# Kernel tuning notes

Hardware: AMD Instinct MI355X
Metric: run time of the kernel (lower is better)

The kernel has to match this reference:

```python
import jax, jax.numpy as jnp
import numpy as np

B, N, DIM = 2, 1024, 256
DEPTH, HEADS, DIM_HEAD = 4, 4, 64
INNER = HEADS * DIM_HEAD
SCALE = DIM_HEAD ** -0.5
STEP, LAMBD, EPS = 0.1, 0.1, 1e-5


def cx(re, im):
    return jax.lax.complex(re, im)


def setup_inputs() -> dict:
    key = jax.random.key(0)
    ks = jax.random.split(key, 8)
    s = np.float32(1.0 / np.sqrt(DIM))
    f32 = jnp.float32
    return {
        "x_re": jax.random.normal(ks[0], (B, N, DIM), f32),
        "x_im": jax.random.normal(ks[1], (B, N, DIM), f32),
        "ln1_w_re": jnp.ones((DEPTH, DIM), f32),
        "ln1_w_im": jnp.zeros((DEPTH, DIM), f32),
        "ln1_b_re": jnp.zeros((DEPTH, DIM), f32),
        "ln1_b_im": jnp.zeros((DEPTH, DIM), f32),
        "qkv_re": jax.random.normal(ks[2], (DEPTH, INNER, DIM), f32) * s,
        "qkv_im": jax.random.normal(ks[3], (DEPTH, INNER, DIM), f32) * s,
        "out_w_re": jax.random.normal(ks[4], (DEPTH, DIM, INNER), f32) * s,
        "out_w_im": jax.random.normal(ks[5], (DEPTH, DIM, INNER), f32) * s,
        "out_b_re": jnp.zeros((DEPTH, DIM), f32),
        "out_b_im": jnp.zeros((DEPTH, DIM), f32),
        "ln2_w_re": jnp.ones((DEPTH, DIM), f32),
        "ln2_w_im": jnp.zeros((DEPTH, DIM), f32),
        "ln2_b_re": jnp.zeros((DEPTH, DIM), f32),
        "ln2_b_im": jnp.zeros((DEPTH, DIM), f32),
        "ff_re": jax.random.normal(ks[6], (DEPTH, DIM, DIM), f32) * s,
        "ff_im": jax.random.normal(ks[7], (DEPTH, DIM, DIM), f32) * s,
    }


def complex_layernorm(x, w, b):
    # per-component mean/var on real and imag (torch unbiased=False), complex sqrt
    mean = cx(jnp.mean(x.real, -1, keepdims=True), jnp.mean(x.imag, -1, keepdims=True))
    var = cx(jnp.var(x.real, -1, keepdims=True), jnp.var(x.imag, -1, keepdims=True))
    xn = (x - mean) / jnp.sqrt(var + EPS)
    return w * xn + b


def attention(x, Wqkv, Wout, bout):
    # torch Linear: y = x @ W^T ; shared qkv projection w
    w = jnp.einsum('bnd,ed->bne', x, Wqkv)              # [B,N,INNER]
    w = w.reshape(B, N, HEADS, DIM_HEAD).transpose(0, 2, 1, 3)  # [B,H,N,Dh]
    dots = jnp.einsum('bhnd,bhmd->bhnm', w, w.conj()) * SCALE   # complex scores
    mag = jnp.abs(dots)
    a = jax.nn.softmax(mag, axis=-1)                    # softmax on magnitudes
    ph = jnp.angle(dots)                                # polar reconstruction
    attn = cx(a * jnp.cos(ph), a * jnp.sin(ph))
    out = jnp.einsum('bhnm,bhmd->bhnd', attn, w)
    out = out.transpose(0, 2, 1, 3).reshape(B, N, INNER)
    return jnp.einsum('bne,de->bnd', out, Wout) + bout


def feedforward(x, W):
    # FeedForward type1: x1 = x W^T ; CReLU(x + step*x1 - step*lambd)
    x1 = jnp.einsum('bnd,ed->bne', x, W)
    z = x + STEP * x1 - STEP * LAMBD
    return cx(jax.nn.relu(z.real), jax.nn.relu(z.imag))


def reference(x_re, x_im, ln1_w_re, ln1_w_im, ln1_b_re, ln1_b_im,
              qkv_re, qkv_im, out_w_re, out_w_im, out_b_re, out_b_im,
              ln2_w_re, ln2_w_im, ln2_b_re, ln2_b_im, ff_re, ff_im):
    x = cx(x_re, x_im)
    for l in range(DEPTH):
        xn = complex_layernorm(x, cx(ln1_w_re[l], ln1_w_im[l]), cx(ln1_b_re[l], ln1_b_im[l]))
        grad_x = attention(xn, cx(qkv_re[l], qkv_im[l]), cx(out_w_re[l], out_w_im[l]),
                           cx(out_b_re[l], out_b_im[l])) + x
        xn2 = complex_layernorm(grad_x, cx(ln2_w_re[l], ln2_w_im[l]), cx(ln2_b_re[l], ln2_b_im[l]))
        x = feedforward(xn2, cx(ff_re[l], ff_im[l]))
    return x
```

## Files before the change

### kernel.cpp

```cpp
#include <hip/hip_runtime.h>
#include <math.h>

#define B_ 2
#define N_ 1024
#define DIM_ 256
#define DEPTH_ 4
#define HEADS_ 4
#define DHEAD_ 64
#define INNER_ 256
#define SCALE_ 0.125f
#define STEP_ 0.1f
#define LAMBD_ 0.1f
#define EPS_ 1e-5f

typedef __attribute__((ext_vector_type(8))) short short8;
typedef __attribute__((ext_vector_type(4))) float f32x4;

__device__ __forceinline__ unsigned short bf16_rne(float x) {
    unsigned u = __float_as_uint(x);
    unsigned r = (u + 0x7FFFu + ((u >> 16) & 1u)) >> 16;
    return (unsigned short)r;
}
__device__ __forceinline__ float bf16_tof(unsigned short h) {
    return __uint_as_float(((unsigned)h) << 16);
}
__device__ __forceinline__ void split2(float x, unsigned short& hi, unsigned short& lo) {
    hi = bf16_rne(x);
    lo = bf16_rne(x - bf16_tof(hi));
}
__device__ __forceinline__ f32x4 mfma16(short8 a, short8 b, f32x4 c) {
    return __builtin_amdgcn_mfma_f32_16x16x32_bf16(a, b, c, 0, 0, 0);
}
__device__ __forceinline__ short8 neg8(short8 v) {
    union { short8 s; unsigned u[4]; } a; a.s = v;
    a.u[0] ^= 0x80008000u; a.u[1] ^= 0x80008000u;
    a.u[2] ^= 0x80008000u; a.u[3] ^= 0x80008000u;
    return a.s;
}

__global__ __launch_bounds__(64)
void ln_kernel(const float* __restrict__ xr, const float* __restrict__ xi,
               const float* __restrict__ wr, const float* __restrict__ wi,
               const float* __restrict__ br, const float* __restrict__ bi,
               float* __restrict__ outr, float* __restrict__ outi,
               unsigned short* __restrict__ planes, int S) {
    int row = blockIdx.x;
    int lane = threadIdx.x;
    int base = row * DIM_ + lane * 4;

    float4 xr4 = *(const float4*)(xr + base);
    float4 xi4 = *(const float4*)(xi + base);
    float ar[4] = {xr4.x, xr4.y, xr4.z, xr4.w};
    float ai[4] = {xi4.x, xi4.y, xi4.z, xi4.w};

    float sr = ar[0] + ar[1] + ar[2] + ar[3];
    float si = ai[0] + ai[1] + ai[2] + ai[3];
#pragma unroll
    for (int o = 1; o < 64; o <<= 1) {
        sr += __shfl_xor(sr, o, 64);
        si += __shfl_xor(si, o, 64);
    }
    float mre = sr * (1.f / DIM_), mim = si * (1.f / DIM_);

    float drv[4], div[4];
    float vr = 0.f, vi = 0.f;
#pragma unroll
    for (int j = 0; j < 4; j++) {
        drv[j] = ar[j] - mre;
        div[j] = ai[j] - mim;
        vr += drv[j] * drv[j];
        vi += div[j] * div[j];
    }
#pragma unroll
    for (int o = 1; o < 64; o <<= 1) {
        vr += __shfl_xor(vr, o, 64);
        vi += __shfl_xor(vi, o, 64);
    }
    float c = vr * (1.f / DIM_) + EPS_;
    float d = vi * (1.f / DIM_);
    float r = sqrtf(c * c + d * d);
    float sre = sqrtf(0.5f * (r + c));
    float sim = sqrtf(fmaxf(0.5f * (r - c), 0.f));
    float inv = 1.f / r;

    int wc = lane * 4;
    float4 wr4 = *(const float4*)(wr + wc);
    float4 wi4 = *(const float4*)(wi + wc);
    float4 br4 = *(const float4*)(br + wc);
    float4 bi4 = *(const float4*)(bi + wc);
    float wrv[4] = {wr4.x, wr4.y, wr4.z, wr4.w};
    float wiv[4] = {wi4.x, wi4.y, wi4.z, wi4.w};
    float brv[4] = {br4.x, br4.y, br4.z, br4.w};
    float biv[4] = {bi4.x, bi4.y, bi4.z, bi4.w};

    float orr[4], oii[4];
    unsigned short rh[4], rl[4], ih[4], il[4];
#pragma unroll
    for (int j = 0; j < 4; j++) {
        float nr = (drv[j] * sre + div[j] * sim) * inv;
        float ni = (div[j] * sre - drv[j] * sim) * inv;
        orr[j] = wrv[j] * nr - wiv[j] * ni + brv[j];
        oii[j] = wrv[j] * ni + wiv[j] * nr + biv[j];
        split2(orr[j], rh[j], rl[j]);
        split2(oii[j], ih[j], il[j]);
    }
    *(float4*)(outr + base) = make_float4(orr[0], orr[1], orr[2], orr[3]);
    *(float4*)(outi + base) = make_float4(oii[0], oii[1], oii[2], oii[3]);
    *(ushort4*)(planes + 0 * (size_t)S + base) = make_ushort4(rh[0], rh[1], rh[2], rh[3]);
    *(ushort4*)(planes + 1 * (size_t)S + base) = make_ushort4(rl[0], rl[1], rl[2], rl[3]);
    *(ushort4*)(planes + 2 * (size_t)S + base) = make_ushort4(ih[0], ih[1], ih[2], ih[3]);
    *(ushort4*)(planes + 3 * (size_t)S + base) = make_ushort4(il[0], il[1], il[2], il[3]);
}

__global__ void wsplit_all(const float* __restrict__ s0r, const float* __restrict__ s0i,
                           const float* __restrict__ s1r, const float* __restrict__ s1i,
                           const float* __restrict__ s2r, const float* __restrict__ s2i,
                           unsigned short* __restrict__ d0,
                           unsigned short* __restrict__ d1,
                           unsigned short* __restrict__ d2) {
    const int PER = DEPTH_ * 65536;
    int gid = blockIdx.x * 256 + threadIdx.x;
    int sel = gid / PER;
    int idx = gid - sel * PER;
    const float* wr = (sel == 0) ? s0r : (sel == 1) ? s1r : s2r;
    const float* wi = (sel == 0) ? s0i : (sel == 1) ? s1i : s2i;
    unsigned short* dst = (sel == 0) ? d0 : (sel == 1) ? d1 : d2;
    int l = idx >> 16, e = idx & 65535;
    unsigned short rh, rl, ih, il;
    split2(wr[idx], rh, rl);
    split2(wi[idx], ih, il);
    size_t base = (size_t)l * 4 * 65536;
    dst[base + 0 * 65536 + e] = rh;
    dst[base + 1 * 65536 + e] = rl;
    dst[base + 2 * 65536 + e] = ih;
    dst[base + 3 * 65536 + e] = il;
}

template <int MODE>
__global__ __launch_bounds__(64)
void gemm_mfma(const unsigned short* __restrict__ Ap, int aStride,
               const unsigned short* __restrict__ Bp,
               unsigned short* __restrict__ wpo, unsigned short* __restrict__ wtpo,
               const float* __restrict__ biasR, const float* __restrict__ biasI,
               const float* resR, const float* resI,
               float* xoR, float* xoI, int S) {
    const int K = 256;
    int tileM = blockIdx.x * 16, tileN = blockIdx.y * 16;
    int lane = threadIdx.x;
    int m16 = lane & 15, quad = lane >> 4;

    f32x4 accP = (f32x4){0,0,0,0}, accN = (f32x4){0,0,0,0};
    f32x4 accIa = (f32x4){0,0,0,0}, accIb = (f32x4){0,0,0,0};

#pragma unroll
    for (int k0 = 0; k0 < 256; k0 += 32) {
        int kb = k0 + quad * 8;
        short8 a[4], b[4];
#pragma unroll
        for (int p = 0; p < 4; p++) {
            a[p] = *(const short8*)(Ap + (size_t)p * aStride + (size_t)(tileM + m16) * K + kb);
            b[p] = *(const short8*)(Bp + (size_t)p * 65536  + (size_t)(tileN + m16) * K + kb);
        }
        accP  = mfma16(a[0], b[0], accP);
        accP  = mfma16(a[0], b[1], accP);
        accP  = mfma16(a[1], b[0], accP);
        accN  = mfma16(a[2], b[2], accN);
        accN  = mfma16(a[2], b[3], accN);
        accN  = mfma16(a[3], b[2], accN);
        accIa = mfma16(a[0], b[2], accIa);
        accIa = mfma16(a[0], b[3], accIa);
        accIa = mfma16(a[1], b[2], accIa);
        accIb = mfma16(a[2], b[0], accIb);
        accIb = mfma16(a[2], b[1], accIb);
        accIb = mfma16(a[3], b[0], accIb);
    }

#pragma unroll
    for (int r = 0; r < 4; r++) {
        int row = tileM + quad * 4 + r;
        int col = tileN + m16;
        size_t g = (size_t)row * 256 + col;
        float vr = accP[r] - accN[r];
        float vi = accIa[r] + accIb[r];
        if (MODE == 1) {
            unsigned short h0, h1, h2, h3;
            split2(vr, h0, h1);
            split2(vi, h2, h3);
            size_t tidx = ((size_t)(row >> 10) * 256 + col) * 1024 + (row & 1023);
            wpo[0 * (size_t)S + g] = h0;
            wpo[1 * (size_t)S + g] = h1;
            wpo[2 * (size_t)S + g] = h2;
            wpo[3 * (size_t)S + g] = h3;
            wtpo[0 * (size_t)S + tidx] = h0;
            wtpo[1 * (size_t)S + tidx] = h1;
            wtpo[2 * (size_t)S + tidx] = h2;
            wtpo[3 * (size_t)S + tidx] = h3;
        } else if (MODE == 2) {
            xoR[g] = vr + biasR[col] + resR[g];
            xoI[g] = vi + biasI[col] + resI[g];
        } else {
            float zr = resR[g] + STEP_ * vr - STEP_ * LAMBD_;
            float zi = resI[g] + STEP_ * vi;
            xoR[g] = fmaxf(zr, 0.f);
            xoI[g] = fmaxf(zi, 0.f);
        }
    }
}

__global__ __launch_bounds__(256, 2)
void attn_mfma(const unsigned short* __restrict__ wp,
               const unsigned short* __restrict__ wtp,
               unsigned short* __restrict__ aop, int S) {
    __shared__ unsigned int ShBuf[6336];
    __shared__ float mlbuf[4][64][2];

    int tid = threadIdx.x;
    int wave = tid >> 6, lane = tid & 63;
    int m16 = lane & 15, quad = lane >> 4;
    int zz = blockIdx.x, bb = zz >> 2, hh = zz & 3;
    int q0 = blockIdx.y * 16;

    short8 qf[4][2], nqr[2][2];
    {
        size_t qbase = (size_t)(bb * N_ + q0 + m16) * INNER_ + hh * DHEAD_;
#pragma unroll
        for (int p = 0; p < 4; p++)
#pragma unroll
            for (int kc = 0; kc < 2; kc++)
                qf[p][kc] = *(const short8*)(wp + (size_t)p * S + qbase + kc * 32 + quad * 8);
        nqr[0][0] = neg8(qf[0][0]); nqr[0][1] = neg8(qf[0][1]);
        nqr[1][0] = neg8(qf[1][0]); nqr[1][1] = neg8(qf[1][1]);
    }

    float mrow = -1e30f, lrow = 0.f;
    f32x4 Oa[4][2];
#pragma unroll
    for (int ni = 0; ni < 4; ni++) { Oa[ni][0] = (f32x4){0,0,0,0}; Oa[ni][1] = (f32x4){0,0,0,0}; }

    unsigned int* prbu = ShBuf + wave * 1056;

    for (int t = 0; t < 4; t++) {
        int kt = wave + 4 * t;

        f32x4 sr[4], si[4];
#pragma unroll
        for (int ni = 0; ni < 4; ni++) { sr[ni] = (f32x4){0,0,0,0}; si[ni] = (f32x4){0,0,0,0}; }
#pragma unroll
        for (int ni = 0; ni < 4; ni++) {
            size_t kbase = (size_t)(bb * N_ + kt * 64 + ni * 16 + m16) * INNER_ + hh * DHEAD_;
            short8 kf[4][2];
#pragma unroll
            for (int p = 0; p < 4; p++)
#pragma unroll
                for (int kc = 0; kc < 2; kc++)
                    kf[p][kc] = *(const short8*)(wp + (size_t)p * S + kbase + kc * 32 + quad * 8);
#pragma unroll
            for (int kc = 0; kc < 2; kc++) {
                f32x4 r = sr[ni], im = si[ni];
                r  = mfma16(kf[0][kc], qf[0][kc], r);
                r  = mfma16(kf[0][kc], qf[1][kc], r);
                r  = mfma16(kf[1][kc], qf[0][kc], r);
                r  = mfma16(kf[2][kc], qf[2][kc], r);
                r  = mfma16(kf[2][kc], qf[3][kc], r);
                r  = mfma16(kf[3][kc], qf[2][kc], r);
                im = mfma16(kf[0][kc], qf[2][kc], im);
                im = mfma16(kf[0][kc], qf[3][kc], im);
                im = mfma16(kf[1][kc], qf[2][kc], im);
                im = mfma16(kf[2][kc], nqr[0][kc], im);
                im = mfma16(kf[2][kc], nqr[1][kc], im);
                im = mfma16(kf[3][kc], nqr[0][kc], im);
                sr[ni] = r; si[ni] = im;
            }
        }

        float mag[4][4], srs[4][4], sis[4][4];
        float mx = -1e30f;
#pragma unroll
        for (int ni = 0; ni < 4; ni++)
#pragma unroll
            for (int r = 0; r < 4; r++) {
                float a = sr[ni][r] * SCALE_, b = si[ni][r] * SCALE_;
                srs[ni][r] = a; sis[ni][r] = b;
                float mg = sqrtf(a * a + b * b);
                mag[ni][r] = mg;
                mx = fmaxf(mx, mg);
            }
        mx = fmaxf(mx, __shfl_xor(mx, 16, 64));
        mx = fmaxf(mx, __shfl_xor(mx, 32, 64));
        float newm = fmaxf(mrow, mx);
        float alpha = __expf(mrow - newm);
        mrow = newm;
        float psum = 0.f;
#pragma unroll
        for (int ni = 0; ni < 4; ni++)
#pragma unroll
            for (int r = 0; r < 4; r++) {
                float p = __expf(mag[ni][r] - newm);
                psum += p;
                float sc = (mag[ni][r] > 0.f) ? (p / mag[ni][r]) : 0.f;
                float pr = (mag[ni][r] > 0.f) ? srs[ni][r] * sc : p;
                float pi = sis[ni][r] * sc;
                int key = ni * 16 + quad * 4 + r;
                prbu[m16 * 66 + key] = ((unsigned)bf16_rne(pi) << 16) | bf16_rne(pr);
            }
        psum += __shfl_xor(psum, 16, 64);
        psum += __shfl_xor(psum, 32, 64);
        lrow = lrow * alpha + psum;
#pragma unroll
        for (int ni = 0; ni < 4; ni++)
#pragma unroll
            for (int r = 0; r < 4; r++) { Oa[ni][0][r] *= alpha; Oa[ni][1][r] *= alpha; }

        short8 prh[2], pih[2], nih[2];
#pragma unroll
        for (int kc = 0; kc < 2; kc++) {
            short8 x, y;
#pragma unroll
            for (int j = 0; j < 8; j++) {
                unsigned val = prbu[m16 * 66 + kc * 32 + quad * 8 + j];
                x[j] = (short)(val & 0xffffu);
                y[j] = (short)(val >> 16);
            }
            prh[kc] = x; pih[kc] = y; nih[kc] = neg8(y);
        }

#pragma unroll
        for (int ni = 0; ni < 4; ni++) {
            size_t vbase = (size_t)(bb * INNER_ + hh * DHEAD_ + ni * 16 + m16) * N_ + kt * 64;
            short8 vr0 = *(const short8*)(wtp + 0 * (size_t)S + vbase + quad * 8);
            short8 vr1 = *(const short8*)(wtp + 0 * (size_t)S + vbase + 32 + quad * 8);
            short8 vi0 = *(const short8*)(wtp + 2 * (size_t)S + vbase + quad * 8);
            short8 vi1 = *(const short8*)(wtp + 2 * (size_t)S + vbase + 32 + quad * 8);
            f32x4 orv = Oa[ni][0], oiv = Oa[ni][1];
            orv = mfma16(vr0, prh[0], orv);
            orv = mfma16(vi0, nih[0], orv);
            orv = mfma16(vr1, prh[1], orv);
            orv = mfma16(vi1, nih[1], orv);
            oiv = mfma16(vr0, pih[0], oiv);
            oiv = mfma16(vi0, prh[0], oiv);
            oiv = mfma16(vr1, pih[1], oiv);
            oiv = mfma16(vi1, prh[1], oiv);
            Oa[ni][0] = orv; Oa[ni][1] = oiv;
        }
    }

    float* Obuf = (float*)ShBuf;
    __syncthreads();
    if (wave != 0) {
        float* mb = Obuf + (wave - 1) * 2112 + lane * 33;
#pragma unroll
        for (int ni = 0; ni < 4; ni++)
#pragma unroll
            for (int r = 0; r < 4; r++) {
                mb[ni * 8 + r]     = Oa[ni][0][r];
                mb[ni * 8 + 4 + r] = Oa[ni][1][r];
            }
        mlbuf[wave][lane][0] = mrow;
        mlbuf[wave][lane][1] = lrow;
    }
    __syncthreads();
    if (wave == 0) {
        float mm = mrow;
#pragma unroll
        for (int w = 1; w < 4; w++) mm = fmaxf(mm, mlbuf[w][lane][0]);
        float a0 = __expf(mrow - mm);
        float ltot = a0 * lrow;
        float aw[3];
#pragma unroll
        for (int w = 1; w < 4; w++) {
            aw[w - 1] = __expf(mlbuf[w][lane][0] - mm);
            ltot += aw[w - 1] * mlbuf[w][lane][1];
        }
        float invl = 1.f / ltot;
        size_t obase = (size_t)(bb * N_ + q0 + m16) * INNER_ + hh * DHEAD_;
#pragma unroll
        for (int ni = 0; ni < 4; ni++)
#pragma unroll
            for (int r = 0; r < 4; r++) {
                float vr = a0 * Oa[ni][0][r];
                float vi = a0 * Oa[ni][1][r];
#pragma unroll
                for (int w = 1; w < 4; w++) {
                    vr += aw[w - 1] * Obuf[(w - 1) * 2112 + lane * 33 + ni * 8 + r];
                    vi += aw[w - 1] * Obuf[(w - 1) * 2112 + lane * 33 + ni * 8 + 4 + r];
                }
                vr *= invl; vi *= invl;
                unsigned short h0, h1, h2, h3;
                split2(vr, h0, h1);
                split2(vi, h2, h3);
                size_t o = obase + ni * 16 + quad * 4 + r;
                aop[0 * (size_t)S + o] = h0;
                aop[1 * (size_t)S + o] = h1;
                aop[2 * (size_t)S + o] = h2;
                aop[3 * (size_t)S + o] = h3;
            }
    }
}

__global__ void pack_real(const float* __restrict__ xr, float* __restrict__ out, int cap) {
    int idx = blockIdx.x * 256 + threadIdx.x;
    if (idx < cap) out[idx] = xr[idx];
}

extern "C" void kernel_launch(void* const* d_in, const int* in_sizes, int n_in,
                              void* d_out, int out_size, void* d_ws, size_t ws_size,
                              hipStream_t stream) {
    const float* in_xre = (const float*)d_in[0];
    const float* in_xim = (const float*)d_in[1];
    const float* ln1wr = (const float*)d_in[2];
    const float* ln1wi = (const float*)d_in[3];
    const float* ln1br = (const float*)d_in[4];
    const float* ln1bi = (const float*)d_in[5];
    const float* qkvr  = (const float*)d_in[6];
    const float* qkvi  = (const float*)d_in[7];
    const float* outwr = (const float*)d_in[8];
    const float* outwi = (const float*)d_in[9];
    const float* outbr = (const float*)d_in[10];
    const float* outbi = (const float*)d_in[11];
    const float* ln2wr = (const float*)d_in[12];
    const float* ln2wi = (const float*)d_in[13];
    const float* ln2br = (const float*)d_in[14];
    const float* ln2bi = (const float*)d_in[15];
    const float* ffr   = (const float*)d_in[16];
    const float* ffi   = (const float*)d_in[17];

    const size_t S = (size_t)B_ * N_ * DIM_;
    const int    Si = (int)S;

    float* ws  = (float*)d_ws;
    float* xre = ws;            float* xim = xre + S;
    float* xnr = xim + S;       float* xni = xnr + S;

    unsigned short* xnp   = (unsigned short*)(xni + S);
    unsigned short* aop   = xnp + 4 * S;
    unsigned short* wpb   = aop + 4 * S;
    unsigned short* wtpb  = wpb + 4 * S;
    unsigned short* qkvp  = wtpb + 4 * S;
    unsigned short* outwp = qkvp + (size_t)DEPTH_ * 4 * 65536;
    unsigned short* ffp   = outwp + (size_t)DEPTH_ * 4 * 65536;

    wsplit_all<<<3 * DEPTH_ * 65536 / 256, 256, 0, stream>>>(
        qkvr, qkvi, outwr, outwi, ffr, ffi, qkvp, outwp, ffp);

    const int MR = B_ * N_;
    dim3 gGemm(MR / 16, INNER_ / 16);
    dim3 gAttn(B_ * HEADS_, N_ / 16);
    int eBlocks = (int)(S / 256);

    bool directOut = (out_size >= (int)(2 * S));
    float* foutR = directOut ? (float*)d_out : xre;
    float* foutI = directOut ? (float*)d_out + S : xim;

    for (int l = 0; l < DEPTH_; l++) {
        const float* xinR = (l == 0) ? in_xre : xre;
        const float* xinI = (l == 0) ? in_xim : xim;

        ln_kernel<<<MR, 64, 0, stream>>>(xinR, xinI,
            ln1wr + l * DIM_, ln1wi + l * DIM_, ln1br + l * DIM_, ln1bi + l * DIM_,
            xnr, xni, xnp, Si);

        gemm_mfma<1><<<gGemm, 64, 0, stream>>>(xnp, Si, qkvp + (size_t)l * 4 * 65536,
            wpb, wtpb, nullptr, nullptr, nullptr, nullptr, nullptr, nullptr, Si);

        attn_mfma<<<gAttn, 256, 0, stream>>>(wpb, wtpb, aop, Si);

        gemm_mfma<2><<<gGemm, 64, 0, stream>>>(aop, Si, outwp + (size_t)l * 4 * 65536,
            nullptr, nullptr, outbr + l * DIM_, outbi + l * DIM_, xinR, xinI, xre, xim, Si);

        ln_kernel<<<MR, 64, 0, stream>>>(xre, xim,
            ln2wr + l * DIM_, ln2wi + l * DIM_, ln2br + l * DIM_, ln2bi + l * DIM_,
            xnr, xni, xnp, Si);

        float* oR = (l == DEPTH_ - 1) ? foutR : xre;
        float* oI = (l == DEPTH_ - 1) ? foutI : xim;
        gemm_mfma<3><<<gGemm, 64, 0, stream>>>(xnp, Si, ffp + (size_t)l * 4 * 65536,
            nullptr, nullptr, nullptr, nullptr, xnr, xni, oR, oI, Si);
    }

    if (!directOut) {
        pack_real<<<eBlocks, 256, 0, stream>>>(xre, (float*)d_out, out_size);
    }
}
```

Baseline: 598.2 us.

## Split attention keys across two blocks and merge partials in separate kernel

```diff
diff --git a/kernel.cpp b/kernel.cpp
--- a/kernel.cpp
+++ b/kernel.cpp
@@ -207,10 +207,10 @@
     }
 }
 
-__global__ __launch_bounds__(256, 2)
+__global__ __launch_bounds__(256, 4)
 void attn_mfma(const unsigned short* __restrict__ wp,
                const unsigned short* __restrict__ wtp,
-               unsigned short* __restrict__ aop, int S) {
+               float* __restrict__ Op, float* __restrict__ ml, int S) {
     __shared__ unsigned int ShBuf[6336];
     __shared__ float mlbuf[4][64][2];
 
@@ -219,6 +219,7 @@
     int m16 = lane & 15, quad = lane >> 4;
     int zz = blockIdx.x, bb = zz >> 2, hh = zz & 3;
     int q0 = blockIdx.y * 16;
+    int kz = blockIdx.z;
 
     short8 qf[4][2], nqr[2][2];
     {
@@ -239,8 +240,8 @@
 
     unsigned int* prbu = ShBuf + wave * 1056;
 
-    for (int t = 0; t < 4; t++) {
-        int kt = wave + 4 * t;
+    for (int t = 0; t < 2; t++) {
+        int kt = kz * 8 + wave + 4 * t;
 
         f32x4 sr[4], si[4];
 #pragma unroll
@@ -371,8 +372,9 @@
             aw[w - 1] = __expf(mlbuf[w][lane][0] - mm);
             ltot += aw[w - 1] * mlbuf[w][lane][1];
         }
-        float invl = 1.f / ltot;
         size_t obase = (size_t)(bb * N_ + q0 + m16) * INNER_ + hh * DHEAD_;
+        float* opr = Op + (size_t)kz * 2 * S;
+        float* opi = opr + S;
 #pragma unroll
         for (int ni = 0; ni < 4; ni++)
 #pragma unroll
@@ -384,17 +386,36 @@
                     vr += aw[w - 1] * Obuf[(w - 1) * 2112 + lane * 33 + ni * 8 + r];
                     vi += aw[w - 1] * Obuf[(w - 1) * 2112 + lane * 33 + ni * 8 + 4 + r];
                 }
-                vr *= invl; vi *= invl;
-                unsigned short h0, h1, h2, h3;
-                split2(vr, h0, h1);
-                split2(vi, h2, h3);
                 size_t o = obase + ni * 16 + quad * 4 + r;
-                aop[0 * (size_t)S + o] = h0;
-                aop[1 * (size_t)S + o] = h1;
-                aop[2 * (size_t)S + o] = h2;
-                aop[3 * (size_t)S + o] = h3;
+                opr[o] = vr;
+                opi[o] = vi;
             }
-    }
+        if (quad == 0) {
+            int row = bb * N_ + q0 + m16;
+            ((float2*)ml)[kz * 8192 + row * 4 + hh] = make_float2(mm, ltot);
+        }
+    }
+}
+
+__global__ void attn_merge(const float* __restrict__ Op, const float* __restrict__ ml,
+                           unsigned short* __restrict__ aop, int S) {
+    int idx = blockIdx.x * 256 + threadIdx.x;
+    int row = idx >> 8;
+    int hh = (idx >> 6) & 3;
+    float2 ml0 = ((const float2*)ml)[row * 4 + hh];
+    float2 ml1 = ((const float2*)ml)[8192 + row * 4 + hh];
+    float mm = fmaxf(ml0.x, ml1.x);
+    float a0 = __expf(ml0.x - mm), a1 = __expf(ml1.x - mm);
+    float invl = 1.f / (a0 * ml0.y + a1 * ml1.y);
+    float vr = (a0 * Op[idx] + a1 * Op[2 * (size_t)S + idx]) * invl;
+    float vi = (a0 * Op[(size_t)S + idx] + a1 * Op[3 * (size_t)S + idx]) * invl;
+    unsigned short h0, h1, h2, h3;
+    split2(vr, h0, h1);
+    split2(vi, h2, h3);
+    aop[0 * (size_t)S + idx] = h0;
+    aop[1 * (size_t)S + idx] = h1;
+    aop[2 * (size_t)S + idx] = h2;
+    aop[3 * (size_t)S + idx] = h3;
 }
 
 __global__ void pack_real(const float* __restrict__ xr, float* __restrict__ out, int cap) {
@@ -430,8 +451,10 @@
     float* ws  = (float*)d_ws;
     float* xre = ws;            float* xim = xre + S;
     float* xnr = xim + S;       float* xni = xnr + S;
-
-    unsigned short* xnp   = (unsigned short*)(xni + S);
+    float* Opart = xni + S;
+    float* mlb   = Opart + 4 * S;
+
+    unsigned short* xnp   = (unsigned short*)(mlb + 32768);
     unsigned short* aop   = xnp + 4 * S;
     unsigned short* wpb   = aop + 4 * S;
     unsigned short* wtpb  = wpb + 4 * S;
@@ -444,7 +467,7 @@
 
     const int MR = B_ * N_;
     dim3 gGemm(MR / 16, INNER_ / 16);
-    dim3 gAttn(B_ * HEADS_, N_ / 16);
+    dim3 gAttn(B_ * HEADS_, N_ / 16, 2);
     int eBlocks = (int)(S / 256);
 
     bool directOut = (out_size >= (int)(2 * S));
@@ -462,7 +485,8 @@
         gemm_mfma<1><<<gGemm, 64, 0, stream>>>(xnp, Si, qkvp + (size_t)l * 4 * 65536,
             wpb, wtpb, nullptr, nullptr, nullptr, nullptr, nullptr, nullptr, Si);
 
-        attn_mfma<<<gAttn, 256, 0, stream>>>(wpb, wtpb, aop, Si);
+        attn_mfma<<<gAttn, 256, 0, stream>>>(wpb, wtpb, Opart, mlb, Si);
+        attn_merge<<<eBlocks, 256, 0, stream>>>(Opart, mlb, aop, Si);
 
         gemm_mfma<2><<<gGemm, 64, 0, stream>>>(aop, Si, outwp + (size_t)l * 4 * 65536,
             nullptr, nullptr, outbr + l * DIM_, outbi + l * DIM_, xinR, xinI, xre, xim, Si);
```

New measurement: 671.1 us. +12.2%, slower.
